# Performance work log

Hardware: AMD Instinct MI355X
Metric: run time of the kernel (lower is better)

Reference implementation:

```python
import jax, jax.numpy as jnp
import numpy as np

HIDDEN = 2048
HEADS = 16
HEAD_DIM = HIDDEN // HEADS
NEG = -10000000000.0

def setup_inputs() -> dict:
    key = jax.random.key(0)
    k1, k2, k3 = jax.random.split(key, 3)
    x = jax.random.normal(k1, (2, 2048, HIDDEN), dtype=jnp.float32)
    # Dense kernels (flax convention: y = x @ W), lecun_normal-ish scaling
    w_qkv = jax.random.normal(k2, (HIDDEN, 3 * HIDDEN), dtype=jnp.float32) / np.sqrt(HIDDEN)
    w_out = jax.random.normal(k3, (HIDDEN, HIDDEN), dtype=jnp.float32) / np.sqrt(HIDDEN)
    return {"x": x, "w_qkv": w_qkv, "w_out": w_out}

def reference(x, w_qkv, w_out):
    b, s, _ = x.shape
    qkv = x @ w_qkv  # [b, s, 3*hidden]
    qkv = qkv.reshape(b, s, 3, HEADS, HEAD_DIM)
    q, k, v = qkv[:, :, 0], qkv[:, :, 1], qkv[:, :, 2]
    scale = jnp.sqrt(jnp.float32(HEAD_DIM)).astype(x.dtype)
    q = q / scale
    scores = jnp.einsum('bqhd,bkhd->bhqk', q, k)  # [b, h, s, s]
    causal_mask = jnp.arange(s)[:, None] >= jnp.arange(s)[None, :]
    scores = jnp.where(causal_mask[None, None], scores, NEG)
    attn = jax.nn.softmax(scores, axis=-1)
    out = jnp.einsum('bhqk,bkhd->bqhd', attn, v).reshape(b, s, HIDDEN)
    return out @ w_out
```

## Files before the change

kernel.cpp:

```cpp
#include <hip/hip_runtime.h>
#include <hip/hip_bf16.h>

typedef __attribute__((ext_vector_type(8))) short bf16x8;
typedef __attribute__((ext_vector_type(4))) float f32x4;
typedef unsigned short ushort_t;

#define HID 2048
#define QKVN 6144
#define SEQ 2048
#define NH 16
#define HD 128
#define QB 128
#define KVB 64

#define GLOBAL_AS __attribute__((address_space(1)))
#define LDS_AS __attribute__((address_space(3)))
typedef LDS_AS const char lds_char;

__device__ __forceinline__ void gload_lds16(const ushort_t* g, ushort_t* l) {
    __builtin_amdgcn_global_load_lds((const GLOBAL_AS unsigned int*)g,
                                     (LDS_AS unsigned int*)l, 16, 0, 0);
}

__device__ __forceinline__ bf16x8 dsr128(lds_char* p) {
    bf16x8 r;
    asm volatile("ds_read_b128 %0, %1" : "=v"(r) : "v"(p));
    return r;
}

__device__ __forceinline__ ushort_t f2b(float f) {
    union { float f; unsigned int u; } x; x.f = f;
    unsigned int r = x.u + 0x7fffu + ((x.u >> 16) & 1u);
    return (ushort_t)(r >> 16);
}

#define BARX() asm volatile("s_barrier" ::: "memory")
#define LGKM0() asm volatile("s_waitcnt lgkmcnt(0)" ::: "memory")
#define VMC0() asm volatile("s_waitcnt vmcnt(0)" ::: "memory")

__global__ __launch_bounds__(256) void castbf(const float* __restrict__ in,
                                              ushort_t* __restrict__ out, int n) {
    int i = (blockIdx.x * 256 + threadIdx.x) * 8;
    if (i >= n) return;
    float4 a = *(const float4*)(in + i);
    float4 b = *(const float4*)(in + i + 4);
    union { ushort_t u[8]; uint4 v; } r;
    r.u[0] = f2b(a.x); r.u[1] = f2b(a.y); r.u[2] = f2b(a.z); r.u[3] = f2b(a.w);
    r.u[4] = f2b(b.x); r.u[5] = f2b(b.y); r.u[6] = f2b(b.z); r.u[7] = f2b(b.w);
    *(uint4*)(out + i) = r.v;
}

__global__ __launch_bounds__(256) void transcast(const float* __restrict__ in,
                                                 ushort_t* __restrict__ out,
                                                 int Kd, int Nd) {
    __shared__ float tile[32][33];
    int tx = threadIdx.x & 31, ty = threadIdx.x >> 5;
    int n0 = blockIdx.x * 32, k0 = blockIdx.y * 32;
    for (int j = 0; j < 4; j++)
        tile[ty + 8 * j][tx] = in[(size_t)(k0 + ty + 8 * j) * Nd + n0 + tx];
    __syncthreads();
    for (int j = 0; j < 4; j++)
        out[(size_t)(n0 + ty + 8 * j) * Kd + k0 + tx] = f2b(tile[tx][ty + 8 * j]);
}

__global__ __launch_bounds__(256) void transV(const ushort_t* __restrict__ qkvb,
                                              ushort_t* __restrict__ vT) {
    __shared__ ushort_t tile[32][33];
    int tx = threadIdx.x & 31, ty = threadIdx.x >> 5;
    int s0 = blockIdx.x * 32, d0 = blockIdx.y * 32;
    int bh = blockIdx.z; int b = bh >> 4, h = bh & 15;
    for (int j = 0; j < 4; j++)
        tile[ty + 8 * j][tx] =
            qkvb[(size_t)(b * SEQ + s0 + ty + 8 * j) * QKVN + 2 * HID + h * HD + d0 + tx];
    __syncthreads();
    for (int j = 0; j < 4; j++)
        vT[((size_t)bh * HD + d0 + ty + 8 * j) * SEQ + s0 + tx] = tile[tx][ty + 8 * j];
}

template <int NFRAG, bool OUT_BF16>
__global__ __launch_bounds__(512, 1) void gemmpl(const ushort_t* __restrict__ A,
                                                 const ushort_t* __restrict__ BT,
                                                 void* __restrict__ C,
                                                 int M, int N, int K,
                                                 int scale_cols, float scale) {
    __shared__ __align__(16) ushort_t As[3][128 * 32];
    __shared__ __align__(16) ushort_t Bs[3][NFRAG * 64 * 32];

    const int t = threadIdx.x;
    const int l = t & 63, w = t >> 6;
    const int wm = w >> 2, wn = w & 3;
    const int lr = l & 15, lg = l >> 4;

    const int nwg = gridDim.x;
    const int cpx = nwg >> 3;
    const int swb = (blockIdx.x & 7) * cpx + (blockIdx.x >> 3);
    const int BN = NFRAG * 64;
    const int NTN = N / BN;
    const int m0 = (swb / NTN) << 7, n0 = (swb % NTN) * BN;

    const int NKT = K >> 5;

    f32x4 acc[4][NFRAG] = {};
    bf16x8 afA[4], bfA[NFRAG], afB[4], bfB[NFRAG];

#define VMCL()                                                                      \
    do { if constexpr (NFRAG == 6) asm volatile("s_waitcnt vmcnt(4)" ::: "memory"); \
         else                      asm volatile("s_waitcnt vmcnt(3)" ::: "memory"); } while (0)
#define VMC2L()                                                                     \
    do { if constexpr (NFRAG == 6) asm volatile("s_waitcnt vmcnt(8)" ::: "memory"); \
         else                      asm volatile("s_waitcnt vmcnt(6)" ::: "memory"); } while (0)

#define STAGE_A(BUF, KT)                                                        \
    do {                                                                        \
        const int r_ = t >> 2, g_ = t & 3;                                      \
        const int gc_ = ((KT) << 5) + ((g_ ^ ((r_ >> 1) & 3)) << 3);            \
        gload_lds16(A + (size_t)(m0 + r_) * K + gc_, &As[BUF][t * 8]);          \
    } while (0)
#define STAGE_B(BUF, KT)                                                        \
    do {                                                                        \
        _Pragma("unroll") for (int sx = 0; sx < NFRAG / 2; sx++) {              \
            const int i_ = sx * 512 + t;                                        \
            const int r_ = i_ >> 2, g_ = i_ & 3;                                \
            const int gc_ = ((KT) << 5) + ((g_ ^ ((r_ >> 1) & 3)) << 3);        \
            gload_lds16(BT + (size_t)(n0 + r_) * K + gc_, &Bs[BUF][i_ * 8]);    \
        }                                                                       \
    } while (0)

#define READS(AF, BF, BI)                                                           \
    do {                                                                            \
        lds_char* aB_ = (lds_char*)&As[BI][0];                                      \
        lds_char* bB_ = (lds_char*)&Bs[BI][0];                                      \
        const int co_ = (lg ^ ((lr >> 1) & 3)) << 4;                                \
        _Pragma("unroll") for (int mi = 0; mi < 4; mi++)                            \
            AF[mi] = dsr128(aB_ + (wm * 64 + mi * 16 + lr) * 64 + co_);             \
        _Pragma("unroll") for (int nj = 0; nj < NFRAG; nj++)                        \
            BF[nj] = dsr128(bB_ + (wn * (NFRAG * 16) + nj * 16 + lr) * 64 + co_);   \
    } while (0)

#define MFMAS(AF, BF)                                                           \
    do {                                                                        \
        __builtin_amdgcn_s_setprio(1);                                          \
        _Pragma("unroll") for (int mi = 0; mi < 4; mi++)                        \
            _Pragma("unroll") for (int nj = 0; nj < NFRAG; nj++)                \
                acc[mi][nj] = __builtin_amdgcn_mfma_f32_16x16x32_bf16(          \
                    AF[mi], BF[nj], acc[mi][nj], 0, 0, 0);                      \
        __builtin_amdgcn_s_setprio(0);                                          \
    } while (0)

#define STEPX(AFU, BFU, AFV, BFV, BI, KT)                                       \
    {                                                                           \
        LGKM0();                                                                \
        __builtin_amdgcn_sched_barrier(0);                                      \
        BARX();                                                                 \
        int nb_ = (BI) + 1; if (nb_ == 3) nb_ = 0;                              \
        READS(AFV, BFV, nb_);                                                   \
        const int st_ = min((KT) + 3, NKT - 1);                                 \
        STAGE_A(BI, st_);                                                       \
        STAGE_B(BI, st_);                                                       \
        VMCL();                                                                 \
        __builtin_amdgcn_sched_barrier(0);                                      \
        MFMAS(AFU, BFU);                                                        \
    }

    STAGE_A(0, 0); STAGE_B(0, 0);
    STAGE_A(1, 1); STAGE_B(1, 1);
    STAGE_A(2, 2); STAGE_B(2, 2);
    VMC2L();
    BARX();
    READS(afA, bfA, 0);
    VMCL();

    int bi = 0;
    for (int kt = 0; kt < NKT; kt += 2) {
        STEPX(afA, bfA, afB, bfB, bi, kt);
        int bi1 = bi + 1; if (bi1 == 3) bi1 = 0;
        STEPX(afB, bfB, afA, bfA, bi1, kt + 1);
        bi += 2; if (bi >= 3) bi -= 3;
    }
    VMC0();

#undef STEPX
#undef MFMAS
#undef READS
#undef STAGE_A
#undef STAGE_B
#undef VMCL
#undef VMC2L

#pragma unroll
    for (int mi = 0; mi < 4; mi++)
#pragma unroll
        for (int nj = 0; nj < NFRAG; nj++) {
            const int row = m0 + wm * 64 + mi * 16 + lg * 4;
            const int col = n0 + wn * (NFRAG * 16) + nj * 16 + lr;
            const float sc = (col < scale_cols) ? scale : 1.0f;
            const f32x4 v = acc[mi][nj];
#pragma unroll
            for (int j = 0; j < 4; j++) {
                if (OUT_BF16)
                    ((ushort_t*)C)[(size_t)(row + j) * N + col] = f2b(v[j] * sc);
                else
                    ((float*)C)[(size_t)(row + j) * N + col] = v[j] * sc;
            }
        }
}

__global__ __launch_bounds__(512, 1) void attn_fwd3(const ushort_t* __restrict__ qkvb,
                                                    const ushort_t* __restrict__ vT,
                                                    ushort_t* __restrict__ attnb) {
    __shared__ __align__(16) ushort_t Ks[2][64 * 128];
    __shared__ __align__(16) ushort_t Vs[2][128 * 64];
    __shared__ __align__(16) ushort_t Ps[8][16 * 64];

    const int t = threadIdx.x;
    const int l = t & 63, w = t >> 6;
    const int lr = l & 15, lg = l >> 4;
    const int pr = blockIdx.x, h = blockIdx.y, b = blockIdx.z;

    const ushort_t* kg = qkvb + (size_t)(b * SEQ) * QKVN + HID + h * HD;
    const ushort_t* vg = vT + (size_t)(b * NH + h) * HD * SEQ;

    char* PsB = (char*)Ps[w];
    const int pssz = ((lr & 7) ^ ((lr >> 3) << 1)) << 4;

    const int kcA = 2 * w, kcB = 2 * w + 1;
    const int krA = 8 * w + (l >> 4), krB = krA + 4;
    const int kcolA = ((l & 15) ^ (l >> 4)) << 3;
    const int kcolB = ((l & 15) ^ (4 + (l >> 4))) << 3;
    const int vrA = 16 * w + (l >> 3), vrB = vrA + 8;
    const int vcol = ((l & 7) ^ (l >> 3)) << 3;

    for (int seg = 0; seg < 2; seg++) {
        const int qt = (seg == 0) ? pr : 15 - pr;
        const int q0 = qt * QB;
        const int q0w = q0 + w * 16;
        const int NT = (q0 + QB) / KVB;

        bf16x8 qf[4];
        {
            const ushort_t* qb = qkvb + (size_t)(b * SEQ + q0w + lr) * QKVN + h * HD + lg * 8;
#pragma unroll
            for (int kc = 0; kc < 4; kc++) qf[kc] = *(const bf16x8*)(qb + kc * 32);
        }
        f32x4 o[8] = {};
        float m[4] = {-3e38f, -3e38f, -3e38f, -3e38f};
        float ls[4] = {0.f, 0.f, 0.f, 0.f};

        __syncthreads();
        gload_lds16(kg + (size_t)krA * QKVN + kcolA, &Ks[0][kcA * 512 + l * 8]);
        gload_lds16(kg + (size_t)krB * QKVN + kcolB, &Ks[0][kcB * 512 + l * 8]);
        gload_lds16(vg + (size_t)vrA * SEQ + vcol,   &Vs[0][kcA * 512 + l * 8]);
        gload_lds16(vg + (size_t)vrB * SEQ + vcol,   &Vs[0][kcB * 512 + l * 8]);

        for (int kt = 0; kt < NT; kt++) {
            const int kv0 = kt * KVB;
            __syncthreads();
            if (kt + 1 < NT) {
                const int nb = (kt + 1) & 1;
                const int nkv = kv0 + KVB;
                gload_lds16(kg + (size_t)(nkv + krA) * QKVN + kcolA, &Ks[nb][kcA * 512 + l * 8]);
                gload_lds16(kg + (size_t)(nkv + krB) * QKVN + kcolB, &Ks[nb][kcB * 512 + l * 8]);
                gload_lds16(vg + (size_t)vrA * SEQ + nkv + vcol,     &Vs[nb][kcA * 512 + l * 8]);
                gload_lds16(vg + (size_t)vrB * SEQ + nkv + vcol,     &Vs[nb][kcB * 512 + l * 8]);
            }
            if (kv0 > q0w + 15) continue;
            const char* KsB = (const char*)Ks[kt & 1];
            const char* VsB = (const char*)Vs[kt & 1];

            f32x4 s[4];
            const int rs = (lr & 7) << 4;
#pragma unroll
            for (int nf = 0; nf < 4; nf++) {
                const int r = nf * 16 + lr;
                s[nf] = (f32x4){0.f, 0.f, 0.f, 0.f};
#pragma unroll
                for (int kc = 0; kc < 4; kc++) {
                    bf16x8 kf = *(const bf16x8*)(KsB + r * 256 + ((kc * 64 + lg * 16) ^ rs));
                    s[nf] = __builtin_amdgcn_mfma_f32_16x16x32_bf16(qf[kc], kf, s[nf], 0, 0, 0);
                }
            }

            const bool diag = (kv0 + 63 > q0w);
            float tm[4];
#pragma unroll
            for (int j = 0; j < 4; j++) {
                if (diag) {
                    const int qpos = q0w + lg * 4 + j;
#pragma unroll
                    for (int nf = 0; nf < 4; nf++)
                        if (kv0 + nf * 16 + lr > qpos) s[nf][j] = -3e38f;
                }
                tm[j] = fmaxf(fmaxf(s[0][j], s[1][j]), fmaxf(s[2][j], s[3][j]));
#pragma unroll
                for (int mk = 1; mk < 16; mk <<= 1)
                    tm[j] = fmaxf(tm[j], __shfl_xor(tm[j], mk, 64));
            }

            float grow = fmaxf(fmaxf(tm[0] - m[0], tm[1] - m[1]),
                               fmaxf(tm[2] - m[2], tm[3] - m[3]));
            if (!__all(grow <= 8.0f)) {
#pragma unroll
                for (int j = 0; j < 4; j++) {
                    const float mn = fmaxf(m[j], tm[j]);
                    const float fac = exp2f((m[j] - mn) * 1.44269504f);
                    m[j] = mn; ls[j] *= fac;
#pragma unroll
                    for (int nf2 = 0; nf2 < 8; nf2++) o[nf2][j] *= fac;
                }
            }

#pragma unroll
            for (int j = 0; j < 4; j++) {
                const int row = lg * 4 + j;
                const int rsz = ((row & 7) ^ ((row >> 3) << 1)) << 4;
                float psum = 0.f;
#pragma unroll
                for (int nf = 0; nf < 4; nf++) {
                    float p = exp2f((s[nf][j] - m[j]) * 1.44269504f);
                    psum += p;
                    union { float f; unsigned u; } cv; cv.f = p;
                    *(ushort_t*)(PsB + row * 128 + ((nf * 32 + lr * 2) ^ rsz)) = (ushort_t)(cv.u >> 16);
                }
                ls[j] += psum;
            }

            bf16x8 pa0 = *(const bf16x8*)(PsB + lr * 128 + ((lg * 16) ^ pssz));
            bf16x8 pa1 = *(const bf16x8*)(PsB + lr * 128 + ((64 + lg * 16) ^ pssz));
#pragma unroll
            for (int nf2 = 0; nf2 < 8; nf2++) {
                const int vr2 = nf2 * 16 + lr;
                bf16x8 vb0 = *(const bf16x8*)(VsB + vr2 * 128 + ((lg * 16) ^ rs));
                bf16x8 vb1 = *(const bf16x8*)(VsB + vr2 * 128 + ((64 + lg * 16) ^ rs));
                o[nf2] = __builtin_amdgcn_mfma_f32_16x16x32_bf16(pa0, vb0, o[nf2], 0, 0, 0);
                o[nf2] = __builtin_amdgcn_mfma_f32_16x16x32_bf16(pa1, vb1, o[nf2], 0, 0, 0);
            }
        }

        float inv[4];
#pragma unroll
        for (int j = 0; j < 4; j++) {
            float sum = ls[j];
#pragma unroll
            for (int mk = 1; mk < 16; mk <<= 1) sum += __shfl_xor(sum, mk, 64);
            inv[j] = 1.0f / sum;
        }
        ushort_t* ob = attnb + (size_t)(b * SEQ + q0w) * HID + h * HD;
#pragma unroll
        for (int nf2 = 0; nf2 < 8; nf2++)
#pragma unroll
            for (int j = 0; j < 4; j++)
                ob[(size_t)(lg * 4 + j) * HID + nf2 * 16 + lr] = f2b(o[nf2][j] * inv[j]);
    }
}

extern "C" void kernel_launch(void* const* d_in, const int* in_sizes, int n_in,
                              void* d_out, int out_size, void* d_ws, size_t ws_size,
                              hipStream_t stream) {
    const float* x     = (const float*)d_in[0];
    const float* w_qkv = (const float*)d_in[1];
    const float* w_out = (const float*)d_in[2];
    float* out = (float*)d_out;

    char* ws = (char*)d_ws;
    ushort_t* xb    = (ushort_t*)(ws);
    ushort_t* wqkvT = (ushort_t*)(ws + 16777216);
    ushort_t* woutT = (ushort_t*)(ws + 41943040);
    ushort_t* qkvb  = (ushort_t*)(ws + 50331648);
    ushort_t* vT    = (ushort_t*)(ws + 100663296);
    ushort_t* attnb = (ushort_t*)(ws + 117440512);

    const int M = 2 * SEQ;

    castbf<<<(M * HID) / (256 * 8), 256, 0, stream>>>(x, xb, M * HID);
    transcast<<<dim3(QKVN / 32, HID / 32), 256, 0, stream>>>(w_qkv, wqkvT, HID, QKVN);
    transcast<<<dim3(HID / 32, HID / 32), 256, 0, stream>>>(w_out, woutT, HID, HID);

    gemmpl<6, true><<<(M / 128) * (QKVN / 384), 512, 0, stream>>>(
        xb, wqkvT, qkvb, M, QKVN, HID, HID, 0.08838834764831845f);

    transV<<<dim3(SEQ / 32, HD / 32, 2 * NH), 256, 0, stream>>>(qkvb, vT);

    attn_fwd3<<<dim3(8, NH, 2), 512, 0, stream>>>(qkvb, vT, attnb);

    gemmpl<4, false><<<(M / 128) * (HID / 256), 512, 0, stream>>>(
        attnb, woutT, out, M, HID, HID, 0, 1.0f);
}
```

Measured before the change: 269.1 us.

## Fuse V transpose into QKV GEMM epilogue and precompute GEMM addressing

```diff
diff --git a/kernel.cpp b/kernel.cpp
--- a/kernel.cpp
+++ b/kernel.cpp
@@ -22,9 +22,10 @@
                                      (LDS_AS unsigned int*)l, 16, 0, 0);
 }
 
-__device__ __forceinline__ bf16x8 dsr128(lds_char* p) {
+template <int OFF>
+__device__ __forceinline__ bf16x8 dsr128o(lds_char* p) {
     bf16x8 r;
-    asm volatile("ds_read_b128 %0, %1" : "=v"(r) : "v"(p));
+    asm volatile("ds_read_b128 %0, %1 offset:%2" : "=v"(r) : "v"(p), "i"(OFF));
     return r;
 }
 
@@ -63,24 +64,11 @@
         out[(size_t)(n0 + ty + 8 * j) * Kd + k0 + tx] = f2b(tile[tx][ty + 8 * j]);
 }
 
-__global__ __launch_bounds__(256) void transV(const ushort_t* __restrict__ qkvb,
-                                              ushort_t* __restrict__ vT) {
-    __shared__ ushort_t tile[32][33];
-    int tx = threadIdx.x & 31, ty = threadIdx.x >> 5;
-    int s0 = blockIdx.x * 32, d0 = blockIdx.y * 32;
-    int bh = blockIdx.z; int b = bh >> 4, h = bh & 15;
-    for (int j = 0; j < 4; j++)
-        tile[ty + 8 * j][tx] =
-            qkvb[(size_t)(b * SEQ + s0 + ty + 8 * j) * QKVN + 2 * HID + h * HD + d0 + tx];
-    __syncthreads();
-    for (int j = 0; j < 4; j++)
-        vT[((size_t)bh * HD + d0 + ty + 8 * j) * SEQ + s0 + tx] = tile[tx][ty + 8 * j];
-}
-
-template <int NFRAG, bool OUT_BF16>
+template <int NFRAG, bool OUT_BF16, bool FUSE_V>
 __global__ __launch_bounds__(512, 1) void gemmpl(const ushort_t* __restrict__ A,
                                                  const ushort_t* __restrict__ BT,
                                                  void* __restrict__ C,
+                                                 ushort_t* __restrict__ vT,
                                                  int M, int N, int K,
                                                  int scale_cols, float scale) {
     __shared__ __align__(16) ushort_t As[3][128 * 32];
@@ -98,10 +86,47 @@
     const int NTN = N / BN;
     const int m0 = (swb / NTN) << 7, n0 = (swb % NTN) * BN;
 
-    const int NKT = K >> 5;
-
     f32x4 acc[4][NFRAG] = {};
     bf16x8 afA[4], bfA[NFRAG], afB[4], bfB[NFRAG];
+
+    const int sr = t >> 2, sg = (t & 3) ^ ((t >> 3) & 3);
+    const ushort_t* aP  = A  + (size_t)(m0 + sr) * K + (sg << 3);
+    const ushort_t* bP0 = BT + (size_t)(n0 + sr) * K + (sg << 3);
+    const ushort_t* bP1 = BT + (size_t)(n0 + 128 + sr) * K + (sg << 3);
+    const ushort_t* bP2 = (NFRAG == 6) ? BT + (size_t)(n0 + 256 + sr) * K + (sg << 3) : nullptr;
+
+    const int co_ = (lg ^ ((lr >> 1) & 3)) << 4;
+    const int aoff = (wm * 64 + lr) * 64 + co_;
+    const int boff = (wn * (NFRAG * 16) + lr) * 64 + co_;
+    lds_char* aR0 = (lds_char*)&As[0][0] + aoff;
+    lds_char* aR1 = (lds_char*)&As[1][0] + aoff;
+    lds_char* aR2 = (lds_char*)&As[2][0] + aoff;
+    lds_char* bR0 = (lds_char*)&Bs[0][0] + boff;
+    lds_char* bR1 = (lds_char*)&Bs[1][0] + boff;
+    lds_char* bR2 = (lds_char*)&Bs[2][0] + boff;
+
+#define GLO(G, L)                                                               \
+    __builtin_amdgcn_global_load_lds((const GLOBAL_AS unsigned int*)(G),        \
+                                     (LDS_AS unsigned int*)(L), 16, 0, 0)
+
+#define STAGES(SB, OFFE)                                                        \
+    do {                                                                        \
+        GLO(aP + (OFFE),  &As[SB][t * 8]);                                      \
+        GLO(bP0 + (OFFE), &Bs[SB][t * 8]);                                      \
+        GLO(bP1 + (OFFE), &Bs[SB][(512 + t) * 8]);                              \
+        if constexpr (NFRAG == 6) GLO(bP2 + (OFFE), &Bs[SB][(1024 + t) * 8]);   \
+    } while (0)
+
+#define READS(AF, BF, AR, BR)                                                   \
+    do {                                                                        \
+        AF[0] = dsr128o<0>(AR);    AF[1] = dsr128o<1024>(AR);                   \
+        AF[2] = dsr128o<2048>(AR); AF[3] = dsr128o<3072>(AR);                   \
+        BF[0] = dsr128o<0>(BR);    BF[1] = dsr128o<1024>(BR);                   \
+        BF[2] = dsr128o<2048>(BR); BF[3] = dsr128o<3072>(BR);                   \
+        if constexpr (NFRAG == 6) {                                             \
+            BF[4] = dsr128o<4096>(BR); BF[5] = dsr128o<5120>(BR);               \
+        }                                                                       \
+    } while (0)
 
 #define VMCL()                                                                      \
     do { if constexpr (NFRAG == 6) asm volatile("s_waitcnt vmcnt(4)" ::: "memory"); \
@@ -109,33 +134,6 @@
 #define VMC2L()                                                                     \
     do { if constexpr (NFRAG == 6) asm volatile("s_waitcnt vmcnt(8)" ::: "memory"); \
          else                      asm volatile("s_waitcnt vmcnt(6)" ::: "memory"); } while (0)
-
-#define STAGE_A(BUF, KT)                                                        \
-    do {                                                                        \
-        const int r_ = t >> 2, g_ = t & 3;                                      \
-        const int gc_ = ((KT) << 5) + ((g_ ^ ((r_ >> 1) & 3)) << 3);            \
-        gload_lds16(A + (size_t)(m0 + r_) * K + gc_, &As[BUF][t * 8]);          \
-    } while (0)
-#define STAGE_B(BUF, KT)                                                        \
-    do {                                                                        \
-        _Pragma("unroll") for (int sx = 0; sx < NFRAG / 2; sx++) {              \
-            const int i_ = sx * 512 + t;                                        \
-            const int r_ = i_ >> 2, g_ = i_ & 3;                                \
-            const int gc_ = ((KT) << 5) + ((g_ ^ ((r_ >> 1) & 3)) << 3);        \
-            gload_lds16(BT + (size_t)(n0 + r_) * K + gc_, &Bs[BUF][i_ * 8]);    \
-        }                                                                       \
-    } while (0)
-
-#define READS(AF, BF, BI)                                                           \
-    do {                                                                            \
-        lds_char* aB_ = (lds_char*)&As[BI][0];                                      \
-        lds_char* bB_ = (lds_char*)&Bs[BI][0];                                      \
-        const int co_ = (lg ^ ((lr >> 1) & 3)) << 4;                                \
-        _Pragma("unroll") for (int mi = 0; mi < 4; mi++)                            \
-            AF[mi] = dsr128(aB_ + (wm * 64 + mi * 16 + lr) * 64 + co_);             \
-        _Pragma("unroll") for (int nj = 0; nj < NFRAG; nj++)                        \
-            BF[nj] = dsr128(bB_ + (wn * (NFRAG * 16) + nj * 16 + lr) * 64 + co_);   \
-    } while (0)
 
 #define MFMAS(AF, BF)                                                           \
     do {                                                                        \
@@ -147,45 +145,54 @@
         __builtin_amdgcn_s_setprio(0);                                          \
     } while (0)
 
-#define STEPX(AFU, BFU, AFV, BFV, BI, KT)                                       \
+#define STEP(SB, AR, BR, AFU, BFU, AFV, BFV, OFFE)                              \
     {                                                                           \
         LGKM0();                                                                \
         __builtin_amdgcn_sched_barrier(0);                                      \
         BARX();                                                                 \
-        int nb_ = (BI) + 1; if (nb_ == 3) nb_ = 0;                              \
-        READS(AFV, BFV, nb_);                                                   \
-        const int st_ = min((KT) + 3, NKT - 1);                                 \
-        STAGE_A(BI, st_);                                                       \
-        STAGE_B(BI, st_);                                                       \
+        READS(AFV, BFV, AR, BR);                                                \
+        STAGES(SB, OFFE);                                                       \
         VMCL();                                                                 \
         __builtin_amdgcn_sched_barrier(0);                                      \
         MFMAS(AFU, BFU);                                                        \
     }
 
-    STAGE_A(0, 0); STAGE_B(0, 0);
-    STAGE_A(1, 1); STAGE_B(1, 1);
-    STAGE_A(2, 2); STAGE_B(2, 2);
+    STAGES(0, 0);
+    STAGES(1, 32);
+    STAGES(2, 64);
+    aP += 96; bP0 += 96; bP1 += 96;
+    if constexpr (NFRAG == 6) bP2 += 96;
     VMC2L();
     BARX();
-    READS(afA, bfA, 0);
+    READS(afA, bfA, aR0, bR0);
     VMCL();
 
-    int bi = 0;
-    for (int kt = 0; kt < NKT; kt += 2) {
-        STEPX(afA, bfA, afB, bfB, bi, kt);
-        int bi1 = bi + 1; if (bi1 == 3) bi1 = 0;
-        STEPX(afB, bfB, afA, bfA, bi1, kt + 1);
-        bi += 2; if (bi >= 3) bi -= 3;
+#pragma unroll 1
+    for (int it = 0; it < 10; it++) {
+        STEP(0, aR1, bR1, afA, bfA, afB, bfB, 0);
+        STEP(1, aR2, bR2, afB, bfB, afA, bfA, 32);
+        STEP(2, aR0, bR0, afA, bfA, afB, bfB, 64);
+        STEP(0, aR1, bR1, afB, bfB, afA, bfA, 96);
+        STEP(1, aR2, bR2, afA, bfA, afB, bfB, 128);
+        STEP(2, aR0, bR0, afB, bfB, afA, bfA, 160);
+        aP += 192; bP0 += 192; bP1 += 192;
+        if constexpr (NFRAG == 6) bP2 += 192;
     }
+    STEP(0, aR1, bR1, afA, bfA, afB, bfB, 0);
+    STEP(1, aR2, bR2, afB, bfB, afA, bfA, 0);
+    STEP(2, aR0, bR0, afA, bfA, afB, bfB, 0);
+    LGKM0();
+    __builtin_amdgcn_sched_barrier(0);
     VMC0();
-
-#undef STEPX
+    MFMAS(afB, bfB);
+
+#undef STEP
 #undef MFMAS
-#undef READS
-#undef STAGE_A
-#undef STAGE_B
 #undef VMCL
 #undef VMC2L
+#undef READS
+#undef STAGES
+#undef GLO
 
 #pragma unroll
     for (int mi = 0; mi < 4; mi++)
@@ -193,14 +200,23 @@
         for (int nj = 0; nj < NFRAG; nj++) {
             const int row = m0 + wm * 64 + mi * 16 + lg * 4;
             const int col = n0 + wn * (NFRAG * 16) + nj * 16 + lr;
-            const float sc = (col < scale_cols) ? scale : 1.0f;
             const f32x4 v = acc[mi][nj];
-#pragma unroll
-            for (int j = 0; j < 4; j++) {
-                if (OUT_BF16)
-                    ((ushort_t*)C)[(size_t)(row + j) * N + col] = f2b(v[j] * sc);
-                else
-                    ((float*)C)[(size_t)(row + j) * N + col] = v[j] * sc;
+            if (FUSE_V && col >= 2 * HID) {
+                const int c = col - 2 * HID;
+                const int b_ = row >> 11, s_ = row & 2047;
+                union { ushort_t u[4]; uint2 q; } pk;
+#pragma unroll
+                for (int j = 0; j < 4; j++) pk.u[j] = f2b(v[j]);
+                *(uint2*)&vT[((size_t)(b_ * NH + (c >> 7)) * HD + (c & 127)) * SEQ + s_] = pk.q;
+            } else {
+                const float sc = (col < scale_cols) ? scale : 1.0f;
+#pragma unroll
+                for (int j = 0; j < 4; j++) {
+                    if (OUT_BF16)
+                        ((ushort_t*)C)[(size_t)(row + j) * N + col] = f2b(v[j] * sc);
+                    else
+                        ((float*)C)[(size_t)(row + j) * N + col] = v[j] * sc;
+                }
             }
         }
 }
@@ -366,8 +382,8 @@
     ushort_t* wqkvT = (ushort_t*)(ws + 16777216);
     ushort_t* woutT = (ushort_t*)(ws + 41943040);
     ushort_t* qkvb  = (ushort_t*)(ws + 50331648);
-    ushort_t* vT    = (ushort_t*)(ws + 100663296);
-    ushort_t* attnb = (ushort_t*)(ws + 117440512);
+    ushort_t* attnb = (ushort_t*)(ws + 100663296);
+    ushort_t* vT    = (ushort_t*)(ws + 117440512);
 
     const int M = 2 * SEQ;
 
@@ -375,13 +391,11 @@
     transcast<<<dim3(QKVN / 32, HID / 32), 256, 0, stream>>>(w_qkv, wqkvT, HID, QKVN);
     transcast<<<dim3(HID / 32, HID / 32), 256, 0, stream>>>(w_out, woutT, HID, HID);
 
-    gemmpl<6, true><<<(M / 128) * (QKVN / 384), 512, 0, stream>>>(
-        xb, wqkvT, qkvb, M, QKVN, HID, HID, 0.08838834764831845f);
-
-    transV<<<dim3(SEQ / 32, HD / 32, 2 * NH), 256, 0, stream>>>(qkvb, vT);
+    gemmpl<6, true, true><<<(M / 128) * (QKVN / 384), 512, 0, stream>>>(
+        xb, wqkvT, qkvb, vT, M, QKVN, HID, HID, 0.08838834764831845f);
 
     attn_fwd3<<<dim3(8, NH, 2), 512, 0, stream>>>(qkvb, vT, attnb);
 
-    gemmpl<4, false><<<(M / 128) * (HID / 256), 512, 0, stream>>>(
-        attnb, woutT, out, M, HID, HID, 0, 1.0f);
-}
+    gemmpl<4, false, false><<<(M / 128) * (HID / 256), 512, 0, stream>>>(
+        attnb, woutT, out, nullptr, M, HID, HID, 0, 1.0f);
+}
```

Measured after the change: 258.4 us. 4.0% less time.
